# Performance work log

Measured on AMD Instinct MI355X. Metric: run time of the kernel, lower is better.

Reference implementation:

```python
import jax, jax.numpy as jnp
import numpy as np

H = 256  # rnn hidden dim per direction

def _lstm_dir(x_proj, w_hh):
    # x_proj: [B, S, 4H] precomputed input projection + bias
    B = x_proj.shape[0]
    def step(carry, xt):
        h, c = carry
        g = xt + h @ w_hh.T  # [B, 4H]
        i, f, gg, o = jnp.split(g, 4, axis=-1)  # torch gate order i,f,g,o
        i = jax.nn.sigmoid(i); f = jax.nn.sigmoid(f)
        gg = jnp.tanh(gg); o = jax.nn.sigmoid(o)
        c = f * c + i * gg
        h = o * jnp.tanh(c)
        return (h, c), h
    h0 = jnp.zeros((B, H), x_proj.dtype)
    _, hs = jax.lax.scan(step, (h0, h0), jnp.swapaxes(x_proj, 0, 1))
    return jnp.swapaxes(hs, 0, 1)  # [B, S, H]

def _bilstm(x, w_ih_f, w_hh_f, b_f, w_ih_b, w_hh_b, b_b):
    hf = _lstm_dir(x @ w_ih_f.T + b_f, w_hh_f)
    hb = _lstm_dir((x @ w_ih_b.T + b_b)[:, ::-1], w_hh_b)[:, ::-1]
    return jnp.concatenate([hf, hb], axis=-1)  # [B, S, 2H]

def _highway(h, hw_W, hw_b):
    proj = h @ hw_W.T + hw_b  # [B, S, 4H]
    nl, gate = jnp.split(proj, 2, axis=-1)
    g = jax.nn.sigmoid(gate)
    return g * h + (1.0 - g) * jax.nn.relu(nl)

def _crf_nll(emit, trans, mask, labels):
    # emit: [B,S,T]; trans[from, to]; START=T-2, STOP=T-1 (NCRF++ convention)
    B, S, T = emit.shape
    START, STOP = T - 2, T - 1
    mb = mask[:, 1:].astype(bool)
    alpha0 = emit[:, 0] + trans[START][None]  # [B,T]
    def step(alpha, inp):
        e_t, m_t = inp
        sc = alpha[:, :, None] + trans[None] + e_t[:, None, :]  # [B,Tprev,Tcur]
        new = jax.nn.logsumexp(sc, axis=1)
        return jnp.where(m_t[:, None], new, alpha), None
    alpha, _ = jax.lax.scan(step, alpha0,
                            (jnp.swapaxes(emit[:, 1:], 0, 1), jnp.swapaxes(mb, 0, 1)))
    fwd_score = jnp.sum(jax.nn.logsumexp(alpha + trans[:, STOP][None], axis=1))
    # gold path score
    prev = jnp.concatenate([jnp.full((B, 1), START, labels.dtype), labels[:, :-1]], axis=1)
    tr = trans[prev, labels]                                       # [B,S]
    em = jnp.take_along_axis(emit, labels[..., None], axis=2)[..., 0]
    lengths = jnp.sum(mask, axis=1)
    last_tag = jnp.take_along_axis(labels, (lengths - 1)[:, None], axis=1)[:, 0]
    gold = jnp.sum((tr + em) * mask.astype(emit.dtype)) + jnp.sum(trans[last_tag, STOP])
    return fwd_score - gold

def _viterbi(emit, trans, mask):
    B, S, T = emit.shape
    START, STOP = T - 2, T - 1
    mb = mask[:, 1:].astype(bool)
    delta0 = emit[:, 0] + trans[START][None]
    iota = jnp.arange(T, dtype=jnp.int32)[None]
    def step(delta, inp):
        e_t, m_t = inp
        sc = delta[:, :, None] + trans[None]     # [B,Tprev,Tcur]
        bp = jnp.argmax(sc, axis=1).astype(jnp.int32)
        best = jnp.max(sc, axis=1) + e_t
        new = jnp.where(m_t[:, None], best, delta)
        bp = jnp.where(m_t[:, None], bp, iota)   # identity at pads -> traceback passes through
        return new, bp
    delta, bps = jax.lax.scan(step, delta0,
                              (jnp.swapaxes(emit[:, 1:], 0, 1), jnp.swapaxes(mb, 0, 1)))
    last = jnp.argmax(delta + trans[:, STOP][None], axis=1).astype(jnp.int32)  # [B]
    def back(tag, bp_t):
        p = jnp.take_along_axis(bp_t, tag[:, None], axis=1)[:, 0]
        return p, p
    _, tags_rev = jax.lax.scan(back, last, bps[::-1])
    tags = jnp.concatenate([tags_rev[::-1], last[None]], axis=0)  # [S,B]
    return jnp.swapaxes(tags, 0, 1) * mask.astype(jnp.int32)


def setup_inputs() -> dict:
    key = jax.random.key(0)
    ks = jax.random.split(key, 16)
    B, S, V, E, L = 64, 512, 32000, 300, 20
    T = L + 2
    lengths = jax.random.randint(ks[0], (B,), S // 4, S + 1)
    input_mask = (jnp.arange(S)[None, :] < lengths[:, None]).astype(jnp.int32)
    word_input = jax.random.randint(ks[1], (B, S), 0, V, dtype=jnp.int32)
    labels = jax.random.randint(ks[2], (B, S), 0, L, dtype=jnp.int32)
    p = lambda k, shp: jax.random.normal(k, shp, dtype=jnp.float32) * 0.1
    return {
        "word_input": word_input, "input_mask": input_mask, "labels": labels,
        "word_emb": p(ks[3], (V, E)),
        "w_ih_f": p(ks[4], (4 * H, E)), "w_hh_f": p(ks[5], (4 * H, H)), "b_f": p(ks[6], (4 * H,)),
        "w_ih_b": p(ks[7], (4 * H, E)), "w_hh_b": p(ks[8], (4 * H, H)), "b_b": p(ks[9], (4 * H,)),
        "hw_W": p(ks[10], (4 * H, 2 * H)),
        "hw_b": jnp.concatenate([p(ks[11], (2 * H,)), jnp.ones((2 * H,), jnp.float32)]),
        "out_W": p(ks[12], (T, 2 * H)), "out_b": p(ks[13], (T,)),
        "trans": p(ks[14], (T, T)),
    }


def reference(word_input, input_mask, labels, word_emb, w_ih_f, w_hh_f, b_f,
              w_ih_b, w_hh_b, b_b, hw_W, hw_b, out_W, out_b, trans):
    B = word_input.shape[0]
    # WordRep (dropout = identity in eval) + mask embeddings
    x = word_emb[word_input] * input_mask[..., None].astype(word_emb.dtype)  # [B,S,E]
    h = _bilstm(x, w_ih_f, w_hh_f, b_f, w_ih_b, w_hh_b, b_b)                 # [B,S,2H]
    h = _highway(h, hw_W, hw_b)
    emit = h @ out_W.T + out_b                                                # [B,S,T]
    nll = _crf_nll(emit, trans, input_mask, labels)
    tag_seq = _viterbi(emit, trans, input_mask)
    return (nll / B, tag_seq)
```

## Files before the change

kernel.cpp:

```cpp
#include <hip/hip_runtime.h>
#include <hip/hip_fp16.h>
#include <math.h>

#define B_  64
#define S_  512
#define E_  300
#define H_  256
#define G4_ 1024
#define T_  22
#define M_  (B_*S_)
#define C_  16
#define NCH (S_/C_)
#define CROWS (B_*C_)
#define RCH 4096
#define START_ (T_-2)
#define STOP_  (T_-1)

__device__ __forceinline__ float sigf(float x){ return 1.f/(1.f+expf(-x)); }

__global__ __launch_bounds__(256) void wtr16_kernel(const float* __restrict__ whh, __half* __restrict__ wT){
  int tid = blockIdx.x*256 + threadIdx.x;
  if (tid >= H_*G4_) return;
  int col = tid >> 8, k = tid & 255;
  int j = col >> 2, gi = col & 3;
  wT[tid] = __float2half(whh[(size_t)(gi*H_ + j)*H_ + k]);
}

struct __align__(16) TileSmem {
  float As[16][68];
  float Bs[16][68];
  int   widx[64];
  float wmsk[64];
};

struct __align__(16) RecSmem {
  __half w[128][268];
  float  hp[4][256];
  float  psum[2][4][32][5];
  float  gbuf[4][4][32];
};

union SmemU { RecSmem r; TileSmem t; };

__device__ __forceinline__ void gemm_tile_body(
    TileSmem& sm, int tid,
    const float* __restrict__ A,
    const int* __restrict__ word, const int* __restrict__ maskp, const float* __restrict__ emb,
    const float* __restrict__ W, const float* __restrict__ bias,
    float* __restrict__ C, int K, int N, int gather, int t0, int chunkC,
    int row0, int col0) {
  const int tn = tid & 15, tm = tid >> 4;
  if (gather) {
    if (tid < 64) {
      int r  = row0 + tid;
      int b  = r / chunkC;
      int tl = r % chunkC;
      int wr = b*S_ + t0 + tl;
      sm.widx[tid] = word[wr];
      sm.wmsk[tid] = (float)maskp[wr];
    }
    __syncthreads();
  }
  float acc[4][4];
  #pragma unroll
  for (int i=0;i<4;i++)
    #pragma unroll
    for (int j=0;j<4;j++) acc[i][j]=0.f;

  for (int k0 = 0; k0 < K; k0 += 16) {
    #pragma unroll
    for (int i = 0; i < 4; ++i) {
      const int li = tid + (i<<8);
      const int m  = li >> 4, kk = li & 15;
      const int kg = k0 + kk;
      float av = 0.f;
      if (kg < K) {
        if (gather) av = emb[(size_t)sm.widx[m]*K + kg] * sm.wmsk[m];
        else        av = A[(size_t)(row0+m)*K + kg];
      }
      sm.As[kk][m] = av;
      const int nc = col0 + m;
      sm.Bs[kk][m] = (kg < K && nc < N) ? W[(size_t)nc*K + kg] : 0.f;
    }
    __syncthreads();
    #pragma unroll
    for (int kk = 0; kk < 16; ++kk) {
      const float4 a = *(const float4*)&sm.As[kk][tm<<2];
      const float4 b = *(const float4*)&sm.Bs[kk][tn<<2];
      acc[0][0]=fmaf(a.x,b.x,acc[0][0]); acc[0][1]=fmaf(a.x,b.y,acc[0][1]);
      acc[0][2]=fmaf(a.x,b.z,acc[0][2]); acc[0][3]=fmaf(a.x,b.w,acc[0][3]);
      acc[1][0]=fmaf(a.y,b.x,acc[1][0]); acc[1][1]=fmaf(a.y,b.y,acc[1][1]);
      acc[1][2]=fmaf(a.y,b.z,acc[1][2]); acc[1][3]=fmaf(a.y,b.w,acc[1][3]);
      acc[2][0]=fmaf(a.z,b.x,acc[2][0]); acc[2][1]=fmaf(a.z,b.y,acc[2][1]);
      acc[2][2]=fmaf(a.z,b.z,acc[2][2]); acc[2][3]=fmaf(a.z,b.w,acc[2][3]);
      acc[3][0]=fmaf(a.w,b.x,acc[3][0]); acc[3][1]=fmaf(a.w,b.y,acc[3][1]);
      acc[3][2]=fmaf(a.w,b.z,acc[3][2]); acc[3][3]=fmaf(a.w,b.w,acc[3][3]);
    }
    __syncthreads();
  }
  #pragma unroll
  for (int i=0;i<4;i++){
    const int r = row0 + (tm<<2) + i;
    #pragma unroll
    for (int j=0;j<4;j++){
      const int c = col0 + (tn<<2) + j;
      if (c < N) C[(size_t)r*N + c] = acc[i][j] + bias[c];
    }
  }
}

__global__ __launch_bounds__(256) void gemm_tiled(
    const float* __restrict__ A,
    const int* __restrict__ word, const int* __restrict__ maskp, const float* __restrict__ emb,
    const float* __restrict__ W, const float* __restrict__ bias,
    float* __restrict__ C, int K, int N, int gather, int t0, int chunkC) {
  __shared__ TileSmem sm;
  gemm_tile_body(sm, threadIdx.x, A, word, maskp, emb, W, bias, C, K, N,
                 gather, t0, chunkC, blockIdx.x << 6, blockIdx.y << 6);
}

__global__ __launch_bounds__(256) void gemm_gates(
    const int* __restrict__ word, const int* __restrict__ maskp, const float* __restrict__ emb,
    const float* __restrict__ w_ih_f, const float* __restrict__ b_f,
    const float* __restrict__ w_ih_b, const float* __restrict__ b_b,
    float* __restrict__ gout, int t0f, int t0b) {
  __shared__ TileSmem sm;
  const int dir = blockIdx.z;
  gemm_tile_body(sm, threadIdx.x, nullptr, word, maskp, emb,
                 dir ? w_ih_b : w_ih_f, dir ? b_b : b_f,
                 gout + (size_t)dir * CROWS * G4_, E_, G4_, 1,
                 dir ? t0b : t0f, C_, blockIdx.x << 6, blockIdx.y << 6);
}

__global__ __launch_bounds__(256) void lstm_mega(
    const float* __restrict__ gcur, float* __restrict__ gnext,
    const int* __restrict__ word, const int* __restrict__ maskp, const float* __restrict__ emb,
    const float* __restrict__ w_ih_f, const float* __restrict__ b_f,
    const float* __restrict__ w_ih_b, const float* __restrict__ b_b,
    const __half* __restrict__ wT16,
    float* __restrict__ h_bi, float* __restrict__ stH, float* __restrict__ stC,
    unsigned long long* __restrict__ hx,
    int t0f, int t0b, int n0f, int n0b, int ebase, int first) {
  __shared__ SmemU sm;
  const int bid = blockIdx.x;
  const int tid = threadIdx.x;

  if (bid >= 256) {
    if (n0f < 0) return;
    #pragma unroll 1
    for (int hfl = 0; hfl < 2; ++hfl) {
      const int tile = (bid - 256)*2 + hfl;
      const int dirg = tile >> 8;
      const int tt   = tile & 255;
      gemm_tile_body(sm.t, tid, nullptr, word, maskp, emb,
                     dirg ? w_ih_b : w_ih_f, dirg ? b_b : b_f,
                     gnext + (size_t)dirg * CROWS * G4_, E_, G4_, 1,
                     dirg ? n0b : n0f, C_, (tt & 15) << 6, (tt >> 4) << 6);
      __syncthreads();
    }
    return;
  }

  const int dir = bid & 1;
  const int cs  = (bid >> 1) & 7;
  const int bq  = bid >> 4;
  const int gidx = dir*16 + bq;
  const float*  __restrict__ g    = gcur + (size_t)dir * CROWS * G4_;
  const __half* __restrict__ wsrc = wT16 + (size_t)dir * (G4_*H_);
  const int hoff = dir ? H_ : 0;

  for (int it = 0; it < 32; ++it) {
    const int idx = tid + (it << 8);
    const int lc = idx >> 6;
    const int k0 = (idx & 63) << 2;
    const uint2 u = *(const uint2*)&wsrc[(size_t)(cs*128 + lc)*256 + k0];
    *(uint2*)&sm.r.w[lc][k0] = u;
  }
  for (int it = 0; it < 4; ++it) {
    const int idx = tid + (it << 8);
    const int b = idx >> 8, col = idx & 255;
    sm.r.hp[b][col] = first ? 0.f : stH[((size_t)(dir*B_ + bq*4 + b))*H_ + col];
  }
  const int ab  = tid >> 5;
  const int ajl = tid & 31;
  float creg = 0.f;
  if (!first && tid < 128)
    creg = stC[((size_t)(dir*B_ + bq*4 + ab))*H_ + cs*32 + ajl];
  __syncthreads();

  const int ks = tid >> 7;
  const int lc = tid & 127;
  const int gi = lc & 3, jl = lc >> 2;
  const int kb = ks << 7;
  const int gb0  = tid >> 7;
  const int grem = tid & 127;
  const int ggi = grem >> 5, gjl = grem & 31;
  const size_t gcol = (size_t)ggi*256 + cs*32 + gjl;

  for (int sl = 0; sl < C_; ++sl) {
    const int t  = dir ? (t0b + C_-1-sl) : (t0f + sl);
    const int tl = dir ? (C_-1-sl) : sl;
    const float gv0 = g[(size_t)((bq*4 + gb0    )*C_ + tl)*G4_ + gcol];
    const float gv1 = g[(size_t)((bq*4 + gb0 + 2)*C_ + tl)*G4_ + gcol];

    float acc0=0.f, acc1=0.f, acc2=0.f, acc3=0.f;
    #pragma unroll 8
    for (int kq = 0; kq < 32; ++kq) {
      const int k0 = kb + (kq << 2);
      const uint2 u = *(const uint2*)&sm.r.w[lc][k0];
      __half2 p01, p23;
      *(unsigned*)&p01 = u.x; *(unsigned*)&p23 = u.y;
      const float2 f01 = __half22float2(p01);
      const float2 f23 = __half22float2(p23);
      const float4 h0 = *(const float4*)&sm.r.hp[0][k0];
      const float4 h1 = *(const float4*)&sm.r.hp[1][k0];
      const float4 h2 = *(const float4*)&sm.r.hp[2][k0];
      const float4 h3 = *(const float4*)&sm.r.hp[3][k0];
      acc0 = fmaf(f01.x,h0.x,fmaf(f01.y,h0.y,fmaf(f23.x,h0.z,fmaf(f23.y,h0.w,acc0))));
      acc1 = fmaf(f01.x,h1.x,fmaf(f01.y,h1.y,fmaf(f23.x,h1.z,fmaf(f23.y,h1.w,acc1))));
      acc2 = fmaf(f01.x,h2.x,fmaf(f01.y,h2.y,fmaf(f23.x,h2.z,fmaf(f23.y,h2.w,acc2))));
      acc3 = fmaf(f01.x,h3.x,fmaf(f01.y,h3.y,fmaf(f23.x,h3.z,fmaf(f23.y,h3.w,acc3))));
    }
    sm.r.psum[ks][gi][jl][0]=acc0; sm.r.psum[ks][gi][jl][1]=acc1;
    sm.r.psum[ks][gi][jl][2]=acc2; sm.r.psum[ks][gi][jl][3]=acc3;
    sm.r.gbuf[gb0    ][ggi][gjl] = gv0;
    sm.r.gbuf[gb0 + 2][ggi][gjl] = gv1;
    __syncthreads();

    const int e = ebase + sl;
    const int par = e & 1;
    const unsigned tag = (unsigned)(e + 1);
    if (tid < 128) {
      const float pre0 = sm.r.gbuf[ab][0][ajl] + sm.r.psum[0][0][ajl][ab] + sm.r.psum[1][0][ajl][ab];
      const float pre1 = sm.r.gbuf[ab][1][ajl] + sm.r.psum[0][1][ajl][ab] + sm.r.psum[1][1][ajl][ab];
      const float pre2 = sm.r.gbuf[ab][2][ajl] + sm.r.psum[0][2][ajl][ab] + sm.r.psum[1][2][ajl][ab];
      const float pre3 = sm.r.gbuf[ab][3][ajl] + sm.r.psum[0][3][ajl][ab] + sm.r.psum[1][3][ajl][ab];
      const float iv = sigf(pre0), fv = sigf(pre1);
      const float zv = tanhf(pre2), ov = sigf(pre3);
      creg = fv*creg + iv*zv;
      const float hn = ov * tanhf(creg);
      h_bi[((size_t)((bq*4+ab)*S_ + t))*(2*H_) + hoff + cs*32 + ajl] = hn;
      if (sl < C_-1) {
        const unsigned long long pk =
            ((unsigned long long)tag << 32) | (unsigned long long)__float_as_uint(hn);
        __hip_atomic_store(&hx[(((size_t)par*32 + gidx)*4 + ab)*256 + cs*32 + ajl], pk,
                           __ATOMIC_RELAXED, __HIP_MEMORY_SCOPE_AGENT);
      } else {
        stH[((size_t)(dir*B_ + bq*4 + ab))*H_ + cs*32 + ajl] = hn;
        stC[((size_t)(dir*B_ + bq*4 + ab))*H_ + cs*32 + ajl] = creg;
      }
    }
    if (sl == C_-1) break;

    {
      const unsigned long long* hb = &hx[((size_t)par*32 + gidx) << 10];
      float r0,r1,r2,r3;
      bool d0=false,d1=false,d2=false,d3=false;
      for (;;) {
        if (!d0) { unsigned long long v = __hip_atomic_load(hb + tid,       __ATOMIC_RELAXED, __HIP_MEMORY_SCOPE_AGENT);
                   if ((unsigned)(v>>32) == tag) { r0 = __uint_as_float((unsigned)v); d0 = true; } }
        if (!d1) { unsigned long long v = __hip_atomic_load(hb + 256 + tid, __ATOMIC_RELAXED, __HIP_MEMORY_SCOPE_AGENT);
                   if ((unsigned)(v>>32) == tag) { r1 = __uint_as_float((unsigned)v); d1 = true; } }
        if (!d2) { unsigned long long v = __hip_atomic_load(hb + 512 + tid, __ATOMIC_RELAXED, __HIP_MEMORY_SCOPE_AGENT);
                   if ((unsigned)(v>>32) == tag) { r2 = __uint_as_float((unsigned)v); d2 = true; } }
        if (!d3) { unsigned long long v = __hip_atomic_load(hb + 768 + tid, __ATOMIC_RELAXED, __HIP_MEMORY_SCOPE_AGENT);
                   if ((unsigned)(v>>32) == tag) { r3 = __uint_as_float((unsigned)v); d3 = true; } }
        if (d0 && d1 && d2 && d3) break;
        __builtin_amdgcn_s_sleep(1);
      }
      sm.r.hp[0][tid] = r0; sm.r.hp[1][tid] = r1;
      sm.r.hp[2][tid] = r2; sm.r.hp[3][tid] = r3;
    }
    __syncthreads();
  }
}

__global__ __launch_bounds__(256) void highway_kernel(
    const float* __restrict__ proj, float* __restrict__ h) {
  int idx = blockIdx.x*256 + threadIdx.x;
  int m = idx >> 9, j = idx & 511;
  float nl = proj[((size_t)m<<10) + j];
  float gt = proj[((size_t)m<<10) + 512 + j];
  float hv = h[idx];
  float gv = sigf(gt);
  h[idx] = gv*hv + (1.f-gv)*fmaxf(nl, 0.f);
}

__global__ __launch_bounds__(256) void gold_kernel(
    const int* __restrict__ labels, const int* __restrict__ maskp,
    const float* __restrict__ emitp, const float* __restrict__ trans, double* __restrict__ gold) {
  const int b = blockIdx.x; const int tid = threadIdx.x;
  double acc = 0.0; int len = 0;
  for (int t = tid; t < S_; t += 256) {
    int mk = maskp[b*S_ + t];
    len += mk;
    if (mk) {
      int lab  = labels[b*S_ + t];
      int prev = (t==0) ? START_ : labels[b*S_ + t - 1];
      acc += (double)trans[prev*T_ + lab] + (double)emitp[((size_t)b*S_ + t)*T_ + lab];
    }
  }
  __shared__ double sacc[256]; __shared__ int slen[256];
  sacc[tid]=acc; slen[tid]=len; __syncthreads();
  for (int s=128; s>0; s>>=1){ if (tid<s){ sacc[tid]+=sacc[tid+s]; slen[tid]+=slen[tid+s]; } __syncthreads(); }
  if (tid==0){
    int L = slen[0];
    int last = labels[b*S_ + L - 1];
    gold[b] = sacc[0] + (double)trans[last*T_ + STOP_];
  }
}

__global__ __launch_bounds__(64) void crf_vit_kernel(
    const float* __restrict__ emitp, const float* __restrict__ trans,
    const int* __restrict__ maskp, double* __restrict__ fwd, float* __restrict__ out_tags) {
  const int b = blockIdx.x;
  const int role = blockIdx.y;
  const int lane = threadIdx.x;
  const int k = lane & 31, p = lane >> 5;
  const int kk = (k < T_) ? k : 0;

  if (role == 0) {
    __shared__ float trs[T_*T_];
    __shared__ double al[T_];
    for (int i = lane; i < T_*T_; i += 64) trs[i] = trans[i];
    __syncthreads();
    if (lane < T_) al[lane] = (double)emitp[(size_t)b*S_*T_ + lane] + (double)trs[START_*T_ + lane];
    __syncthreads();
    float ce = emitp[((size_t)b*S_ + 1)*T_ + kk];
    int   cm = maskp[b*S_ + 1];
    for (int t = 1; t < S_; ++t) {
      float ne = 0.f; int nm = 0;
      if (t+1 < S_) { ne = emitp[((size_t)b*S_ + t + 1)*T_ + kk]; nm = maskp[b*S_ + t + 1]; }
      double tj[11];
      #pragma unroll
      for (int u = 0; u < 11; ++u) {
        const int j = p*11 + u;
        tj[u] = al[j] + (double)trs[j*T_ + kk];
      }
      double m = tj[0];
      #pragma unroll
      for (int u = 1; u < 11; ++u) m = fmax(m, tj[u]);
      m = fmax(m, __shfl_xor(m, 32));
      float s = 0.f;
      #pragma unroll
      for (int u = 0; u < 11; ++u) s += __expf((float)(tj[u] - m));
      s += __shfl_xor(s, 32);
      const double nv = m + (double)__logf(s) + (double)ce;
      __syncthreads();
      if (cm && p == 0 && k < T_) al[k] = nv;
      __syncthreads();
      ce = ne; cm = nm;
    }
    if (lane == 0) {
      double mx = -1e300;
      for (int j = 0; j < T_; ++j) mx = fmax(mx, al[j] + (double)trs[j*T_ + STOP_]);
      double s = 0.0;
      for (int j = 0; j < T_; ++j) s += exp(al[j] + (double)trs[j*T_ + STOP_] - mx);
      fwd[b] = mx + log(s);
    }
  } else {
    __shared__ double tr64[T_*T_];
    __shared__ double dl[T_];
    __shared__ unsigned char bp[S_][T_];
    __shared__ int msk[S_];
    for (int i = lane; i < T_*T_; i += 64) tr64[i] = (double)trans[i];
    __syncthreads();
    if (lane < T_) dl[lane] = (double)emitp[(size_t)b*S_*T_ + lane] + tr64[START_*T_ + lane];
    if (lane == 0) msk[0] = maskp[b*S_];
    __syncthreads();
    float ce = emitp[((size_t)b*S_ + 1)*T_ + kk];
    int   cm = maskp[b*S_ + 1];
    for (int t = 1; t < S_; ++t) {
      float ne = 0.f; int nm = 0;
      if (t+1 < S_) { ne = emitp[((size_t)b*S_ + t + 1)*T_ + kk]; nm = maskp[b*S_ + t + 1]; }
      double best = dl[p*11] + tr64[(p*11)*T_ + kk];
      int arg = p*11;
      #pragma unroll
      for (int u = 1; u < 11; ++u) {
        const int j = p*11 + u;
        const double sc = dl[j] + tr64[j*T_ + kk];
        if (sc > best) { best = sc; arg = j; }
      }
      const double ob = __shfl_xor(best, 32);
      const int    oa = __shfl_xor(arg, 32);
      if (p == 0 && ob > best) { best = ob; arg = oa; }
      __syncthreads();
      if (p == 0 && k < T_) {
        if (cm) { dl[k] = best + (double)ce; bp[t][k] = (unsigned char)arg; }
        else    { bp[t][k] = (unsigned char)k; }
      }
      if (lane == 0) msk[t] = cm;
      __syncthreads();
      ce = ne; cm = nm;
    }
    if (lane == 0) {
      double bb = dl[0] + tr64[STOP_]; int cur = 0;
      for (int j = 1; j < T_; ++j) { const double sc = dl[j] + tr64[j*T_ + STOP_]; if (sc > bb) { bb = sc; cur = j; } }
      for (int t = S_-1; ; --t) {
        out_tags[b*S_ + t] = (float)(cur * msk[t]);
        if (t == 0) break;
        cur = bp[t][cur];
      }
    }
  }
}

__global__ void finalize_kernel(const double* __restrict__ fwd, const double* __restrict__ gold, float* __restrict__ out){
  if (threadIdx.x == 0 && blockIdx.x == 0) {
    double s = 0.0, g = 0.0;
    for (int b = 0; b < B_; ++b) { s += fwd[b]; g += gold[b]; }
    out[0] = (float)((s - g) / (double)B_);
  }
}

extern "C" void kernel_launch(void* const* d_in, const int* in_sizes, int n_in,
                              void* d_out, int out_size, void* d_ws, size_t ws_size,
                              hipStream_t stream) {
  const int*   word   = (const int*)d_in[0];
  const int*   maskp  = (const int*)d_in[1];
  const int*   labels = (const int*)d_in[2];
  const float* emb    = (const float*)d_in[3];
  const float* w_ih_f = (const float*)d_in[4];
  const float* w_hh_f = (const float*)d_in[5];
  const float* b_f    = (const float*)d_in[6];
  const float* w_ih_b = (const float*)d_in[7];
  const float* w_hh_b = (const float*)d_in[8];
  const float* b_b    = (const float*)d_in[9];
  const float* hw_W   = (const float*)d_in[10];
  const float* hw_b   = (const float*)d_in[11];
  const float* out_W  = (const float*)d_in[12];
  const float* out_b  = (const float*)d_in[13];
  const float* trans  = (const float*)d_in[14];
  float* out = (float*)d_out;

  float* h_bi  = (float*)d_ws;
  float* buf0  = h_bi + 16777216ULL;
  float* buf1  = buf0 + 2097152ULL;
  __half* wT16 = (__half*)(buf1 + 2097152ULL);
  float* emitp = (float*)(wT16 + 524288ULL);
  float* stH   = emitp + 720896ULL;
  float* stC   = stH + 32768ULL;
  unsigned long long* hx = (unsigned long long*)(stC + 32768ULL);
  double* fwdp = (double*)(hx + 65536ULL);
  double* goldp = fwdp + 64;

  hipMemsetAsync(hx, 0, 65536ULL * 8, stream);

  wtr16_kernel<<<1024, 256, 0, stream>>>(w_hh_f, wT16);
  wtr16_kernel<<<1024, 256, 0, stream>>>(w_hh_b, wT16 + 262144ULL);

  gemm_gates<<<dim3(CROWS/64, 16, 2), 256, 0, stream>>>(
      word, maskp, emb, w_ih_f, b_f, w_ih_b, b_b, buf0, 0, S_ - C_);

  for (int i = 0; i < NCH; ++i) {
    const int t0f = i * C_;
    const int t0b = S_ - (i + 1) * C_;
    const int n0f = (i < NCH-1) ? (i + 1) * C_ : -1;
    const int n0b = S_ - (i + 2) * C_;
    float* gcur = (i & 1) ? buf1 : buf0;
    float* gnext = (i & 1) ? buf0 : buf1;
    lstm_mega<<<512, 256, 0, stream>>>(
        gcur, gnext, word, maskp, emb, w_ih_f, b_f, w_ih_b, b_b,
        wT16, h_bi, stH, stC, hx, t0f, t0b, n0f, n0b, i*(C_-1), (i == 0) ? 1 : 0);
  }

  for (int rc = 0; rc < M_ / RCH; ++rc) {
    float* Ach = h_bi + (size_t)rc * RCH * 512;
    gemm_tiled<<<dim3(RCH/64, 16), 256, 0, stream>>>(
        Ach, nullptr, nullptr, nullptr, hw_W, hw_b, buf0, 2*H_, G4_, 0, 0, C_);
    highway_kernel<<<(RCH*512)/256, 256, 0, stream>>>(buf0, Ach);
  }

  gemm_tiled<<<dim3(M_/64, 1), 256, 0, stream>>>(
      h_bi, nullptr, nullptr, nullptr, out_W, out_b, emitp, 2*H_, T_, 0, 0, C_);

  gold_kernel<<<64, 256, 0, stream>>>(labels, maskp, emitp, trans, goldp);
  crf_vit_kernel<<<dim3(64, 2), 64, 0, stream>>>(emitp, trans, maskp, fwdp, out + 1);
  finalize_kernel<<<1, 64, 0, stream>>>(fwdp, goldp, out);
}
```

Baseline: 4.469 ms.

## Keep recurrent LSTM weights in registers and split K across 8 warps

The recurrent weight slice moves from shared-memory fp16 tiles into per-thread fp32 registers (128 floats per thread), and the K dimension is split across 8 wavefront groups with a wider partial-sum reduction. The block also raises wave priority, uses fast exp-based sigmoid and tanh, and writes its own h slice directly to shared memory, so the wavefront owning that segment skips polling the exchange buffer. The goal is to remove per-step LDS weight reads and half-to-float conversions on the latency-critical recurrence. In exchange, register pressure rises sharply with a risk of spills, and the fast transcendentals reduce accuracy slightly.

```diff
diff --git a/kernel.cpp b/kernel.cpp
--- a/kernel.cpp
+++ b/kernel.cpp
@@ -16,7 +16,8 @@
 #define START_ (T_-2)
 #define STOP_  (T_-1)
 
-__device__ __forceinline__ float sigf(float x){ return 1.f/(1.f+expf(-x)); }
+__device__ __forceinline__ float sigf(float x){ return 1.f/(1.f+__expf(-x)); }
+__device__ __forceinline__ float tanhfast(float x){ float e=__expf(2.f*x); return 1.f - 2.f/(e+1.f); }
 
 __global__ __launch_bounds__(256) void wtr16_kernel(const float* __restrict__ whh, __half* __restrict__ wT){
   int tid = blockIdx.x*256 + threadIdx.x;
@@ -34,9 +35,8 @@
 };
 
 struct __align__(16) RecSmem {
-  __half w[128][268];
   float  hp[4][256];
-  float  psum[2][4][32][5];
+  float  psum[8][4][32][5];
   float  gbuf[4][4][32];
 };
 
@@ -161,6 +161,7 @@
     return;
   }
 
+  __builtin_amdgcn_s_setprio(1);
   const int dir = bid & 1;
   const int cs  = (bid >> 1) & 7;
   const int bq  = bid >> 4;
@@ -169,13 +170,25 @@
   const __half* __restrict__ wsrc = wT16 + (size_t)dir * (G4_*H_);
   const int hoff = dir ? H_ : 0;
 
-  for (int it = 0; it < 32; ++it) {
-    const int idx = tid + (it << 8);
-    const int lc = idx >> 6;
-    const int k0 = (idx & 63) << 2;
-    const uint2 u = *(const uint2*)&wsrc[(size_t)(cs*128 + lc)*256 + k0];
-    *(uint2*)&sm.r.w[lc][k0] = u;
-  }
+  const int lc4 = tid & 31;
+  const int ks  = tid >> 5;
+  const int kb  = ks << 5;
+  const int colg0 = cs*128 + (lc4 << 2);
+
+  float wreg[4][32];
+  #pragma unroll
+  for (int i = 0; i < 4; ++i) {
+    const __half* base = wsrc + (size_t)(colg0 + i)*256 + kb;
+    #pragma unroll
+    for (int q = 0; q < 16; ++q) {
+      const __half2 hh = *(const __half2*)(base + q*2);
+      const float2 f = __half22float2(hh);
+      wreg[i][q*2]   = f.x;
+      wreg[i][q*2+1] = f.y;
+    }
+  }
+
+  #pragma unroll
   for (int it = 0; it < 4; ++it) {
     const int idx = tid + (it << 8);
     const int b = idx >> 8, col = idx & 255;
@@ -186,16 +199,13 @@
   float creg = 0.f;
   if (!first && tid < 128)
     creg = stC[((size_t)(dir*B_ + bq*4 + ab))*H_ + cs*32 + ajl];
-  __syncthreads();
-
-  const int ks = tid >> 7;
-  const int lc = tid & 127;
-  const int gi = lc & 3, jl = lc >> 2;
-  const int kb = ks << 7;
+
   const int gb0  = tid >> 7;
   const int grem = tid & 127;
   const int ggi = grem >> 5, gjl = grem & 31;
   const size_t gcol = (size_t)ggi*256 + cs*32 + gjl;
+  const bool ownseg = ((tid >> 5) == cs);
+  __syncthreads();
 
   for (int sl = 0; sl < C_; ++sl) {
     const int t  = dir ? (t0b + C_-1-sl) : (t0f + sl);
@@ -203,26 +213,35 @@
     const float gv0 = g[(size_t)((bq*4 + gb0    )*C_ + tl)*G4_ + gcol];
     const float gv1 = g[(size_t)((bq*4 + gb0 + 2)*C_ + tl)*G4_ + gcol];
 
-    float acc0=0.f, acc1=0.f, acc2=0.f, acc3=0.f;
-    #pragma unroll 8
-    for (int kq = 0; kq < 32; ++kq) {
+    float4 acc[4];
+    #pragma unroll
+    for (int i=0;i<4;++i) acc[i] = make_float4(0.f,0.f,0.f,0.f);
+    #pragma unroll
+    for (int kq = 0; kq < 8; ++kq) {
       const int k0 = kb + (kq << 2);
-      const uint2 u = *(const uint2*)&sm.r.w[lc][k0];
-      __half2 p01, p23;
-      *(unsigned*)&p01 = u.x; *(unsigned*)&p23 = u.y;
-      const float2 f01 = __half22float2(p01);
-      const float2 f23 = __half22float2(p23);
       const float4 h0 = *(const float4*)&sm.r.hp[0][k0];
       const float4 h1 = *(const float4*)&sm.r.hp[1][k0];
       const float4 h2 = *(const float4*)&sm.r.hp[2][k0];
       const float4 h3 = *(const float4*)&sm.r.hp[3][k0];
-      acc0 = fmaf(f01.x,h0.x,fmaf(f01.y,h0.y,fmaf(f23.x,h0.z,fmaf(f23.y,h0.w,acc0))));
-      acc1 = fmaf(f01.x,h1.x,fmaf(f01.y,h1.y,fmaf(f23.x,h1.z,fmaf(f23.y,h1.w,acc1))));
-      acc2 = fmaf(f01.x,h2.x,fmaf(f01.y,h2.y,fmaf(f23.x,h2.z,fmaf(f23.y,h2.w,acc2))));
-      acc3 = fmaf(f01.x,h3.x,fmaf(f01.y,h3.y,fmaf(f23.x,h3.z,fmaf(f23.y,h3.w,acc3))));
-    }
-    sm.r.psum[ks][gi][jl][0]=acc0; sm.r.psum[ks][gi][jl][1]=acc1;
-    sm.r.psum[ks][gi][jl][2]=acc2; sm.r.psum[ks][gi][jl][3]=acc3;
+      #pragma unroll
+      for (int i = 0; i < 4; ++i) {
+        const float w0 = wreg[i][(kq<<2)+0];
+        const float w1 = wreg[i][(kq<<2)+1];
+        const float w2 = wreg[i][(kq<<2)+2];
+        const float w3 = wreg[i][(kq<<2)+3];
+        acc[i].x = fmaf(w0,h0.x,fmaf(w1,h0.y,fmaf(w2,h0.z,fmaf(w3,h0.w,acc[i].x))));
+        acc[i].y = fmaf(w0,h1.x,fmaf(w1,h1.y,fmaf(w2,h1.z,fmaf(w3,h1.w,acc[i].y))));
+        acc[i].z = fmaf(w0,h2.x,fmaf(w1,h2.y,fmaf(w2,h2.z,fmaf(w3,h2.w,acc[i].z))));
+        acc[i].w = fmaf(w0,h3.x,fmaf(w1,h3.y,fmaf(w2,h3.z,fmaf(w3,h3.w,acc[i].w))));
+      }
+    }
+    #pragma unroll
+    for (int i = 0; i < 4; ++i) {
+      sm.r.psum[ks][i][lc4][0] = acc[i].x;
+      sm.r.psum[ks][i][lc4][1] = acc[i].y;
+      sm.r.psum[ks][i][lc4][2] = acc[i].z;
+      sm.r.psum[ks][i][lc4][3] = acc[i].w;
+    }
     sm.r.gbuf[gb0    ][ggi][gjl] = gv0;
     sm.r.gbuf[gb0 + 2][ggi][gjl] = gv1;
     __syncthreads();
@@ -231,14 +250,22 @@
     const int par = e & 1;
     const unsigned tag = (unsigned)(e + 1);
     if (tid < 128) {
-      const float pre0 = sm.r.gbuf[ab][0][ajl] + sm.r.psum[0][0][ajl][ab] + sm.r.psum[1][0][ajl][ab];
-      const float pre1 = sm.r.gbuf[ab][1][ajl] + sm.r.psum[0][1][ajl][ab] + sm.r.psum[1][1][ajl][ab];
-      const float pre2 = sm.r.gbuf[ab][2][ajl] + sm.r.psum[0][2][ajl][ab] + sm.r.psum[1][2][ajl][ab];
-      const float pre3 = sm.r.gbuf[ab][3][ajl] + sm.r.psum[0][3][ajl][ab] + sm.r.psum[1][3][ajl][ab];
+      float pre0 = sm.r.gbuf[ab][0][ajl];
+      float pre1 = sm.r.gbuf[ab][1][ajl];
+      float pre2 = sm.r.gbuf[ab][2][ajl];
+      float pre3 = sm.r.gbuf[ab][3][ajl];
+      #pragma unroll
+      for (int k2 = 0; k2 < 8; ++k2) {
+        pre0 += sm.r.psum[k2][0][ajl][ab];
+        pre1 += sm.r.psum[k2][1][ajl][ab];
+        pre2 += sm.r.psum[k2][2][ajl][ab];
+        pre3 += sm.r.psum[k2][3][ajl][ab];
+      }
       const float iv = sigf(pre0), fv = sigf(pre1);
-      const float zv = tanhf(pre2), ov = sigf(pre3);
+      const float zv = tanhfast(pre2), ov = sigf(pre3);
       creg = fv*creg + iv*zv;
-      const float hn = ov * tanhf(creg);
+      const float hn = ov * tanhfast(creg);
+      sm.r.hp[ab][cs*32 + ajl] = hn;
       h_bi[((size_t)((bq*4+ab)*S_ + t))*(2*H_) + hoff + cs*32 + ajl] = hn;
       if (sl < C_-1) {
         const unsigned long long pk =
@@ -252,7 +279,7 @@
     }
     if (sl == C_-1) break;
 
-    {
+    if (!ownseg) {
       const unsigned long long* hb = &hx[((size_t)par*32 + gidx) << 10];
       float r0,r1,r2,r3;
       bool d0=false,d1=false,d2=false,d3=false;
```

Result: slower. 5.732 ms (+28.3%).

## Fuse highway GEMM with gating epilogue and keep CRF state in registers

Applied to the files above, without the earlier changes.

Replaces the chunked highway GEMM plus separate elementwise kernel with one kernel. Each block computes a 32-row strip across all 1024 projection columns and applies the sigmoid/relu gating in place, so the projection never goes to global memory. The CRF forward and Viterbi loops now keep alpha/delta in registers and broadcast them with wave shuffles instead of shared memory and two barriers per step, with transition values cached in registers. The fused GEMM needs a large shared tile and 128 accumulators per thread, which can lower occupancy. It launches only 1024 blocks and reloads the whole weight matrix for every row strip.

```diff
diff --git a/kernel.cpp b/kernel.cpp
--- a/kernel.cpp
+++ b/kernel.cpp
@@ -12,7 +12,6 @@
 #define C_  16
 #define NCH (S_/C_)
 #define CROWS (B_*C_)
-#define RCH 4096
 #define START_ (T_-2)
 #define STOP_  (T_-1)
 
@@ -130,6 +129,75 @@
                  dir ? w_ih_b : w_ih_f, dir ? b_b : b_f,
                  gout + (size_t)dir * CROWS * G4_, E_, G4_, 1,
                  dir ? t0b : t0f, C_, blockIdx.x << 6, blockIdx.y << 6);
+}
+
+__global__ __launch_bounds__(256) void gemm_hw_full(
+    float* __restrict__ h, const float* __restrict__ hwW, const float* __restrict__ hwb) {
+  __shared__ __align__(16) float As[16][36];
+  __shared__ __align__(16) float Bs[16][1024];
+  const int tid = threadIdx.x;
+  const int cg  = tid & 63;
+  const int rg  = tid >> 6;
+  const int row0 = blockIdx.x << 5;
+  const int r0 = rg << 3;
+  float an[8][8], ag[8][8];
+  #pragma unroll
+  for (int i=0;i<8;++i)
+    #pragma unroll
+    for (int u=0;u<8;++u){ an[i][u]=0.f; ag[i][u]=0.f; }
+
+  for (int k0 = 0; k0 < 512; k0 += 16) {
+    #pragma unroll
+    for (int it = 0; it < 2; ++it) {
+      const int e = tid + (it << 8);
+      const int rr = e >> 4, kk = e & 15;
+      As[kk][rr] = h[(size_t)(row0 + rr)*512 + k0 + kk];
+    }
+    #pragma unroll
+    for (int it = 0; it < 16; ++it) {
+      const int e = tid + (it << 8);
+      const int c  = e >> 2;
+      const int kq = (e & 3) << 2;
+      const float4 v = *(const float4*)&hwW[(size_t)c*512 + k0 + kq];
+      Bs[kq+0][c] = v.x; Bs[kq+1][c] = v.y; Bs[kq+2][c] = v.z; Bs[kq+3][c] = v.w;
+    }
+    __syncthreads();
+    #pragma unroll 4
+    for (int kk = 0; kk < 16; ++kk) {
+      const float4 a0 = *(const float4*)&As[kk][r0];
+      const float4 a1 = *(const float4*)&As[kk][r0+4];
+      const float ar[8] = {a0.x,a0.y,a0.z,a0.w,a1.x,a1.y,a1.z,a1.w};
+      float bn[8], bg[8];
+      #pragma unroll
+      for (int u = 0; u < 8; ++u) {
+        bn[u] = Bs[kk][cg + (u<<6)];
+        bg[u] = Bs[kk][512 + cg + (u<<6)];
+      }
+      #pragma unroll
+      for (int i = 0; i < 8; ++i)
+        #pragma unroll
+        for (int u = 0; u < 8; ++u) {
+          an[i][u] = fmaf(ar[i], bn[u], an[i][u]);
+          ag[i][u] = fmaf(ar[i], bg[u], ag[i][u]);
+        }
+    }
+    __syncthreads();
+  }
+  #pragma unroll
+  for (int u = 0; u < 8; ++u) {
+    const int c = cg + (u<<6);
+    const float bn_ = hwb[c];
+    const float bg_ = hwb[512 + c];
+    #pragma unroll
+    for (int i = 0; i < 8; ++i) {
+      const size_t off = (size_t)(row0 + r0 + i)*512 + c;
+      const float nl = an[i][u] + bn_;
+      const float gt = ag[i][u] + bg_;
+      const float hv = h[off];
+      const float gv = sigf(gt);
+      h[off] = gv*hv + (1.f-gv)*fmaxf(nl, 0.f);
+    }
+  }
 }
 
 __global__ __launch_bounds__(256) void lstm_mega(
@@ -275,17 +343,6 @@
   }
 }
 
-__global__ __launch_bounds__(256) void highway_kernel(
-    const float* __restrict__ proj, float* __restrict__ h) {
-  int idx = blockIdx.x*256 + threadIdx.x;
-  int m = idx >> 9, j = idx & 511;
-  float nl = proj[((size_t)m<<10) + j];
-  float gt = proj[((size_t)m<<10) + 512 + j];
-  float hv = h[idx];
-  float gv = sigf(gt);
-  h[idx] = gv*hv + (1.f-gv)*fmaxf(nl, 0.f);
-}
-
 __global__ __launch_bounds__(256) void gold_kernel(
     const int* __restrict__ labels, const int* __restrict__ maskp,
     const float* __restrict__ emitp, const float* __restrict__ trans, double* __restrict__ gold) {
@@ -319,13 +376,17 @@
   const int k = lane & 31, p = lane >> 5;
   const int kk = (k < T_) ? k : 0;
 
+  __shared__ float trs[T_*T_];
+  for (int i = lane; i < T_*T_; i += 64) trs[i] = trans[i];
+  __syncthreads();
+
+  float trreg[11];
+  #pragma unroll
+  for (int u = 0; u < 11; ++u) trreg[u] = trs[(p*11 + u)*T_ + kk];
+
   if (role == 0) {
-    __shared__ float trs[T_*T_];
-    __shared__ double al[T_];
-    for (int i = lane; i < T_*T_; i += 64) trs[i] = trans[i];
-    __syncthreads();
-    if (lane < T_) al[lane] = (double)emitp[(size_t)b*S_*T_ + lane] + (double)trs[START_*T_ + lane];
-    __syncthreads();
+    double al_r = 0.0;
+    if (lane < T_) al_r = (double)emitp[(size_t)b*S_*T_ + lane] + (double)trs[START_*T_ + lane];
     float ce = emitp[((size_t)b*S_ + 1)*T_ + kk];
     int   cm = maskp[b*S_ + 1];
     for (int t = 1; t < S_; ++t) {
@@ -333,10 +394,8 @@
       if (t+1 < S_) { ne = emitp[((size_t)b*S_ + t + 1)*T_ + kk]; nm = maskp[b*S_ + t + 1]; }
       double tj[11];
       #pragma unroll
-      for (int u = 0; u < 11; ++u) {
-        const int j = p*11 + u;
-        tj[u] = al[j] + (double)trs[j*T_ + kk];
-      }
+      for (int u = 0; u < 11; ++u)
+        tj[u] = __shfl(al_r, p*11 + u) + (double)trreg[u];
       double m = tj[0];
       #pragma unroll
       for (int u = 1; u < 11; ++u) m = fmax(m, tj[u]);
@@ -346,56 +405,52 @@
       for (int u = 0; u < 11; ++u) s += __expf((float)(tj[u] - m));
       s += __shfl_xor(s, 32);
       const double nv = m + (double)__logf(s) + (double)ce;
-      __syncthreads();
-      if (cm && p == 0 && k < T_) al[k] = nv;
-      __syncthreads();
+      if (cm && lane < T_) al_r = nv;
       ce = ne; cm = nm;
     }
-    if (lane == 0) {
-      double mx = -1e300;
-      for (int j = 0; j < T_; ++j) mx = fmax(mx, al[j] + (double)trs[j*T_ + STOP_]);
-      double s = 0.0;
-      for (int j = 0; j < T_; ++j) s += exp(al[j] + (double)trs[j*T_ + STOP_] - mx);
-      fwd[b] = mx + log(s);
-    }
+    if (lane < T_) al_r += (double)trs[lane*T_ + STOP_];
+    double mx = (lane < T_) ? al_r : -1e300;
+    #pragma unroll
+    for (int o = 32; o > 0; o >>= 1) mx = fmax(mx, __shfl_xor(mx, o));
+    double sv = (lane < T_) ? exp(al_r - mx) : 0.0;
+    #pragma unroll
+    for (int o = 32; o > 0; o >>= 1) sv += __shfl_xor(sv, o);
+    if (lane == 0) fwd[b] = mx + log(sv);
   } else {
-    __shared__ double tr64[T_*T_];
-    __shared__ double dl[T_];
     __shared__ unsigned char bp[S_][T_];
     __shared__ int msk[S_];
-    for (int i = lane; i < T_*T_; i += 64) tr64[i] = (double)trans[i];
-    __syncthreads();
-    if (lane < T_) dl[lane] = (double)emitp[(size_t)b*S_*T_ + lane] + tr64[START_*T_ + lane];
+    double dl_r = 0.0;
+    if (lane < T_) dl_r = (double)emitp[(size_t)b*S_*T_ + lane] + (double)trs[START_*T_ + lane];
     if (lane == 0) msk[0] = maskp[b*S_];
-    __syncthreads();
     float ce = emitp[((size_t)b*S_ + 1)*T_ + kk];
     int   cm = maskp[b*S_ + 1];
     for (int t = 1; t < S_; ++t) {
       float ne = 0.f; int nm = 0;
       if (t+1 < S_) { ne = emitp[((size_t)b*S_ + t + 1)*T_ + kk]; nm = maskp[b*S_ + t + 1]; }
-      double best = dl[p*11] + tr64[(p*11)*T_ + kk];
+      double best = __shfl(dl_r, p*11) + (double)trreg[0];
       int arg = p*11;
       #pragma unroll
       for (int u = 1; u < 11; ++u) {
-        const int j = p*11 + u;
-        const double sc = dl[j] + tr64[j*T_ + kk];
-        if (sc > best) { best = sc; arg = j; }
+        const double sc = __shfl(dl_r, p*11 + u) + (double)trreg[u];
+        if (sc > best) { best = sc; arg = p*11 + u; }
       }
       const double ob = __shfl_xor(best, 32);
       const int    oa = __shfl_xor(arg, 32);
       if (p == 0 && ob > best) { best = ob; arg = oa; }
-      __syncthreads();
       if (p == 0 && k < T_) {
-        if (cm) { dl[k] = best + (double)ce; bp[t][k] = (unsigned char)arg; }
+        if (cm) { dl_r = best + (double)ce; bp[t][k] = (unsigned char)arg; }
         else    { bp[t][k] = (unsigned char)k; }
       }
       if (lane == 0) msk[t] = cm;
-      __syncthreads();
       ce = ne; cm = nm;
     }
+    __syncthreads();
     if (lane == 0) {
-      double bb = dl[0] + tr64[STOP_]; int cur = 0;
-      for (int j = 1; j < T_; ++j) { const double sc = dl[j] + tr64[j*T_ + STOP_]; if (sc > bb) { bb = sc; cur = j; } }
+      double bb = -1e300; int cur = 0;
+      for (int j = T_-1; j >= 0; --j) {
+        const double sc = __shfl(dl_r, j) + (double)trs[j*T_ + STOP_];
+        if (sc >= bb) { bb = sc; cur = j; }
+      }
       for (int t = S_-1; ; --t) {
         out_tags[b*S_ + t] = (float)(cur * msk[t]);
         if (t == 0) break;
@@ -464,12 +519,7 @@
         wT16, h_bi, stH, stC, hx, t0f, t0b, n0f, n0b, i*(C_-1), (i == 0) ? 1 : 0);
   }
 
-  for (int rc = 0; rc < M_ / RCH; ++rc) {
-    float* Ach = h_bi + (size_t)rc * RCH * 512;
-    gemm_tiled<<<dim3(RCH/64, 16), 256, 0, stream>>>(
-        Ach, nullptr, nullptr, nullptr, hw_W, hw_b, buf0, 2*H_, G4_, 0, 0, C_);
-    highway_kernel<<<(RCH*512)/256, 256, 0, stream>>>(buf0, Ach);
-  }
+  gemm_hw_full<<<M_/32, 256, 0, stream>>>(h_bi, hw_W, hw_b);
 
   gemm_tiled<<<dim3(M_/64, 1), 256, 0, stream>>>(
       h_bi, nullptr, nullptr, nullptr, out_W, out_b, emitp, 2*H_, T_, 0, 0, C_);
```

Result: faster. 4.236 ms (-5.2%).
